# Performance work log

Hardware: AMD Instinct MI355X
Metric: run time of the kernel (lower is better)

The kernel has to match this reference:

```python
import jax, jax.numpy as jnp
import numpy as np
from jax import lax

B, S, V, E, H, L, LAT = 32, 64, 32000, 128, 512, 2, 64

def setup_inputs() -> dict:
    key = jax.random.key(0)
    ks = jax.random.split(key, 40)
    sc = 0.05
    inputs = jax.random.randint(ks[0], (B, S), 0, V, dtype=jnp.int32)
    lengths = jnp.sort(jax.random.randint(ks[1], (B,), 1, S + 1, dtype=jnp.int32))[::-1]
    lengths = lengths.at[0].set(S)  # enforce_sorted=True, max length == S for static shapes
    d = {
        'inputs': inputs,
        'lengths': lengths,
        'noise': jax.random.normal(ks[2], (L, B, LAT), jnp.float32),
        'embed_table': jax.random.normal(ks[3], (V, E), jnp.float32) * sc,
        'enc_Wm': jax.random.normal(ks[4], (LAT, E), jnp.float32) * sc,
        'enc_bm': jnp.zeros((LAT,), jnp.float32),
        'enc_Wv': jax.random.normal(ks[5], (LAT, E), jnp.float32) * sc,
        'enc_bv': jnp.zeros((LAT,), jnp.float32),
        'W_l2r': jax.random.normal(ks[6], (H, LAT), jnp.float32) * sc,
        'b_l2r': jnp.zeros((H,), jnp.float32),
        'gru_Wih0': jax.random.normal(ks[7], (3 * H, E), jnp.float32) * sc,
        'gru_Whh0': jax.random.normal(ks[8], (3 * H, H), jnp.float32) * sc,
        'gru_bih0': jnp.zeros((3 * H,), jnp.float32),
        'gru_bhh0': jnp.zeros((3 * H,), jnp.float32),
        'gru_Wih1': jax.random.normal(ks[9], (3 * H, H), jnp.float32) * sc,
        'gru_Whh1': jax.random.normal(ks[10], (3 * H, H), jnp.float32) * sc,
        'gru_bih1': jnp.zeros((3 * H,), jnp.float32),
        'gru_bhh1': jnp.zeros((3 * H,), jnp.float32),
        'W_out': jax.random.normal(ks[11], (V, H), jnp.float32) * sc,
        'b_out': jnp.zeros((V,), jnp.float32),
        'logp_W1': jax.random.normal(ks[12], (200, LAT), jnp.float32) * sc,
        'logp_b1': jnp.zeros((200,), jnp.float32),
        'logp_W2': jax.random.normal(ks[13], (100, 200), jnp.float32) * sc,
        'logp_b2': jnp.zeros((100,), jnp.float32),
        'logp_W3': jax.random.normal(ks[14], (1, 100), jnp.float32) * sc,
        'logp_b3': jnp.zeros((1,), jnp.float32),
        'sas_W1': jax.random.normal(ks[15], (200, LAT), jnp.float32) * sc,
        'sas_b1': jnp.zeros((200,), jnp.float32),
        'sas_W2': jax.random.normal(ks[16], (100, 200), jnp.float32) * sc,
        'sas_b2': jnp.zeros((100,), jnp.float32),
        'sas_W3': jax.random.normal(ks[17], (1, 100), jnp.float32) * sc,
        'sas_b3': jnp.zeros((1,), jnp.float32),
    }
    return d

def _gru_layer(x, h0, Wih, Whh, bih, bhh, lengths):
    # x: [B,T,D]; PyTorch GRU gate order: r, z, n. Packed semantics: state frozen
    # and output zero beyond each sample's length.
    T = x.shape[1]
    xW = jnp.einsum('btd,gd->btg', x, Wih) + bih          # [B,T,3H] one big GEMM
    tmask = jnp.arange(T)[:, None] < lengths[None, :]      # [T,B]
    def step(h, inp):
        xw_t, m_t = inp                                    # [B,3H], [B]
        hW = h @ Whh.T + bhh
        xr, xz, xn = jnp.split(xw_t, 3, axis=-1)
        hr, hz, hn = jnp.split(hW, 3, axis=-1)
        r = jax.nn.sigmoid(xr + hr)
        u = jax.nn.sigmoid(xz + hz)
        n = jnp.tanh(xn + r * hn)
        h_new = (1.0 - u) * n + u * h
        m = m_t[:, None]
        h = jnp.where(m, h_new, h)
        out = jnp.where(m, h_new, 0.0)
        return h, out
    hT, outs = lax.scan(step, h0, (xW.transpose(1, 0, 2), tmask))
    return outs.transpose(1, 0, 2), hT                     # [B,T,H], [B,H]

def _mlp3(x, W1, b1, W2, b2, W3, b3):
    h = jax.nn.relu(x @ W1.T + b1)
    h = jax.nn.relu(h @ W2.T + b2)
    return (h @ W3.T + b3).reshape(-1)

def reference(inputs, lengths, noise, embed_table, enc_Wm, enc_bm, enc_Wv, enc_bv,
              W_l2r, b_l2r, gru_Wih0, gru_Whh0, gru_bih0, gru_bhh0,
              gru_Wih1, gru_Whh1, gru_bih1, gru_bhh1, W_out, b_out,
              logp_W1, logp_b1, logp_W2, logp_b2, logp_W3, logp_b3,
              sas_W1, sas_b1, sas_W2, sas_b2, sas_W3, sas_b3):
    emb = embed_table[inputs]                              # [B,S,E] gather
    # ragged masked segment-sum: sum embeddings of tokens with id > 2 per sample
    mask = (inputs > 2)[..., None].astype(emb.dtype)
    vec_frag = jnp.sum(emb * mask, axis=1)                 # [B,E]
    mean = vec_frag @ enc_Wm.T + enc_bm                    # [B,LAT]
    logv = vec_frag @ enc_Wv.T + enc_bv
    std = jnp.exp(0.5 * logv)
    z = noise * std + mean                                 # [L,B,LAT]
    pred_logp = _mlp3(mean, logp_W1, logp_b1, logp_W2, logp_b2, logp_W3, logp_b3)
    pred_sas = _mlp3(mean, sas_W1, sas_b1, sas_W2, sas_b2, sas_W3, sas_b3)
    state = z @ W_l2r.T + b_l2r                            # [L,B,H]
    # decoder: 2-layer GRU (eval mode: no dropout), then vocab projection
    out0, _ = _gru_layer(emb, state[0], gru_Wih0, gru_Whh0, gru_bih0, gru_bhh0, lengths)
    out1, _ = _gru_layer(out0, state[1], gru_Wih1, gru_Whh1, gru_bih1, gru_bhh1, lengths)
    output = out1 @ W_out.T + b_out                        # [B,S,V]
    return (output, mean, std, z, pred_logp, pred_sas)
```

## Files before the change

### kernel.cpp

```cpp
#include <hip/hip_runtime.h>


typedef __attribute__((ext_vector_type(8))) short bf16x8_t;
typedef __attribute__((ext_vector_type(8))) unsigned short u16x8_t;
typedef __attribute__((ext_vector_type(4))) float f32x4_t;
typedef __attribute__((ext_vector_type(8))) _Float16 f16x8_t;
typedef __attribute__((ext_vector_type(4))) unsigned int u32x4_t;

#define AS_AGENT __HIP_MEMORY_SCOPE_AGENT

static __device__ __forceinline__ unsigned short f2bf(float f) {
    unsigned int u = __float_as_uint(f);
    u += 0x7fffu + ((u >> 16) & 1u);
    return (unsigned short)(u >> 16);
}
static __device__ __forceinline__ unsigned short bfround(unsigned int u) {
    u += 0x7fffu + ((u >> 16) & 1u);
    return (unsigned short)(u >> 16);
}
static __device__ __forceinline__ unsigned short f2h(float f) {
    _Float16 h = (_Float16)f;
    return __builtin_bit_cast(unsigned short, h);
}
static __device__ __forceinline__ float sigmoidf_(float x) {
    return 1.f / (1.f + __expf(-x));
}

__global__ __launch_bounds__(256) void embed_encoder_kernel(
    const int* __restrict__ tok, const float* __restrict__ table,
    const float* __restrict__ Wih0f,
    const float* __restrict__ Wm, const float* __restrict__ bm,
    const float* __restrict__ Wv, const float* __restrict__ bv,
    const float* __restrict__ noise,
    const float* __restrict__ Wl2r, const float* __restrict__ bl2r,
    const float* __restrict__ lW1, const float* __restrict__ lb1,
    const float* __restrict__ lW2, const float* __restrict__ lb2,
    const float* __restrict__ lW3, const float* __restrict__ lb3,
    const float* __restrict__ sW1, const float* __restrict__ sb1,
    const float* __restrict__ sW2, const float* __restrict__ sb2,
    const float* __restrict__ sW3, const float* __restrict__ sb3,
    float* __restrict__ o_mean, float* __restrict__ o_std, float* __restrict__ o_z,
    float* __restrict__ o_logp, float* __restrict__ o_sas,
    float* __restrict__ state,
    unsigned short* __restrict__ embb,
    unsigned short* __restrict__ Wih0b)
{
    const int b = blockIdx.x, tid = threadIdx.x;
    __shared__ float v_[128], mn[64], sd[64], zz[2][64], hh1[200], hh2[100];
    if (tid < 128) {
        const int e = tid;
        float acc = 0.f;
        for (int s = 0; s < 64; ++s) {
            int id = tok[b * 64 + s];
            float v = table[(size_t)id * 128 + e];
            embb[(size_t)(b * 64 + s) * 128 + e] = f2bf(v);
            if (id > 2) acc += v;
        }
        v_[e] = acc;
    }
    for (int i = b * 256 + tid; i < 49152; i += 8192) {
        float4 v = reinterpret_cast<const float4*>(Wih0f)[i];
        ushort4 o;
        o.x = f2bf(v.x); o.y = f2bf(v.y); o.z = f2bf(v.z); o.w = f2bf(v.w);
        reinterpret_cast<ushort4*>(Wih0b)[i] = o;
    }
    __syncthreads();
    if (tid < 128) {
        int j = tid & 63;
        bool isv = tid >= 64;
        const float* W = (isv ? Wv : Wm) + j * 128;
        float a = isv ? bv[j] : bm[j];
#pragma unroll 4
        for (int k = 0; k < 128; ++k) a = fmaf(v_[k], W[k], a);
        if (!isv) { mn[j] = a; o_mean[b * 64 + j] = a; }
        else      { float s = __expf(0.5f * a); sd[j] = s; o_std[b * 64 + j] = s; }
    }
    __syncthreads();
    if (tid < 128) {
        int l = tid >> 6, j = tid & 63;
        float zv = fmaf(noise[(l * 32 + b) * 64 + j], sd[j], mn[j]);
        zz[l][j] = zv;
        o_z[(l * 32 + b) * 64 + j] = zv;
    }
    __syncthreads();
#pragma unroll
    for (int p = 0; p < 4; ++p) {
        int tt = p * 256 + tid;
        int l = tt >> 9, hd = tt & 511;
        const float* W = Wl2r + hd * 64;
        float a = bl2r[hd];
#pragma unroll 4
        for (int k = 0; k < 64; ++k) a = fmaf(zz[l][k], W[k], a);
        state[(size_t)(l * 32 + b) * 512 + hd] = a;
    }
    if (tid < 200) {
        const float* W = lW1 + tid * 64;
        float a = lb1[tid];
        for (int k = 0; k < 64; ++k) a = fmaf(mn[k], W[k], a);
        hh1[tid] = fmaxf(a, 0.f);
    }
    __syncthreads();
    if (tid < 100) {
        const float* W = lW2 + tid * 200;
        float a = lb2[tid];
        for (int k = 0; k < 200; ++k) a = fmaf(hh1[k], W[k], a);
        hh2[tid] = fmaxf(a, 0.f);
    }
    __syncthreads();
    if (tid == 0) {
        float a = lb3[0];
        for (int k = 0; k < 100; ++k) a = fmaf(hh2[k], lW3[k], a);
        o_logp[b] = a;
    }
    __syncthreads();
    if (tid < 200) {
        const float* W = sW1 + tid * 64;
        float a = sb1[tid];
        for (int k = 0; k < 64; ++k) a = fmaf(mn[k], W[k], a);
        hh1[tid] = fmaxf(a, 0.f);
    }
    __syncthreads();
    if (tid < 100) {
        const float* W = sW2 + tid * 200;
        float a = sb2[tid];
        for (int k = 0; k < 200; ++k) a = fmaf(hh1[k], W[k], a);
        hh2[tid] = fmaxf(a, 0.f);
    }
    __syncthreads();
    if (tid == 0) {
        float a = sb3[0];
        for (int k = 0; k < 100; ++k) a = fmaf(hh2[k], sW3[k], a);
        o_sas[b] = a;
    }
}

#define NWG_L0 16
#define NWG_TOT 48
#define NWG_ALL 256
#define NWG_GEMM 208
#define OCH 32832

__global__ __launch_bounds__(512) void gru_fused_kernel(
    float* __restrict__ xW0,
    const unsigned short* __restrict__ embb,
    const unsigned short* __restrict__ Wih0b,
    const float* __restrict__ bih0,
    const float* __restrict__ Whh0, const float* __restrict__ bhh0,
    const float* __restrict__ Whh1, const float* __restrict__ Wih1,
    const float* __restrict__ bih1, const float* __restrict__ bhh1,
    const float* __restrict__ hinit,
    const int* __restrict__ lengths,
    unsigned short* __restrict__ h0x,
    unsigned short* __restrict__ h1x,
    unsigned short* __restrict__ o0x,
    unsigned short* __restrict__ out1x,
    const float* __restrict__ Woutf,
    unsigned short* __restrict__ Woutb,
    const float* __restrict__ bout,
    float* __restrict__ outp,
    int* __restrict__ flags)
{
    __shared__ __align__(16) char smem[157184];
    const int tid = threadIdx.x;
    const int wg = blockIdx.x;
    const int lane = tid & 63;
    const int wave = tid >> 6;
    unsigned int* __restrict__ h0x32 = (unsigned int*)h0x;
    unsigned int* __restrict__ h1x32 = (unsigned int*)h1x;
    unsigned int* __restrict__ o0x32 = (unsigned int*)o0x;
    unsigned int* __restrict__ o1x32 = (unsigned int*)out1x;

    (void)__hip_atomic_load(&flags[0], __ATOMIC_ACQUIRE, AS_AGENT);

    if (wg >= NWG_TOT) {
        unsigned short* lA = (unsigned short*)smem;
        unsigned short* lB = (unsigned short*)(smem + 16384);
        const int g = wg - NWG_TOT;
        const int wm = wave >> 2;
        const int wn = wave & 3;

        if (g < 192) {
            const int pm = g / 12, pn = g % 12;
            f32x4_t pacc[4][2];
#pragma unroll
            for (int i = 0; i < 4; ++i)
#pragma unroll
                for (int j = 0; j < 2; ++j) pacc[i][j] = (f32x4_t){0.f, 0.f, 0.f, 0.f};
            for (int kt = 0; kt < 128; kt += 64) {
#pragma unroll
                for (int p = 0; p < 2; ++p) {
                    int gi = p * 512 + tid;
                    int row = gi >> 3, c8 = gi & 7;
                    int dst = row * 64 + ((c8 ^ (row & 7)) << 3);
                    *(u32x4_t*)&lA[dst] = *(const u32x4_t*)(embb +
                        (size_t)(pm * 128 + row) * 128 + kt + (c8 << 3));
                    *(u32x4_t*)&lB[dst] = *(const u32x4_t*)(Wih0b +
                        (size_t)(pn * 128 + row) * 128 + kt + (c8 << 3));
                }
                __syncthreads();
#pragma unroll
                for (int kc = 0; kc < 2; ++kc) {
                    int c8 = kc * 4 + (lane >> 4);
                    bf16x8_t af[4], bfr[2];
#pragma unroll
                    for (int i = 0; i < 4; ++i) {
                        int ra = wm * 64 + i * 16 + (lane & 15);
                        af[i] = *(const bf16x8_t*)&lA[ra * 64 + ((c8 ^ (ra & 7)) << 3)];
                    }
#pragma unroll
                    for (int j = 0; j < 2; ++j) {
                        int rb = wn * 32 + j * 16 + (lane & 15);
                        bfr[j] = *(const bf16x8_t*)&lB[rb * 64 + ((c8 ^ (rb & 7)) << 3)];
                    }
#pragma unroll
                    for (int i = 0; i < 4; ++i)
#pragma unroll
                        for (int j = 0; j < 2; ++j)
                            pacc[i][j] = __builtin_amdgcn_mfma_f32_16x16x32_bf16(
                                af[i], bfr[j], pacc[i][j], 0, 0, 0);
                }
                __syncthreads();
            }
            const int lm = (lane >> 4) * 4, ln = lane & 15;
#pragma unroll
            for (int i = 0; i < 4; ++i) {
#pragma unroll
                for (int j = 0; j < 2; ++j) {
                    int gn = pn * 128 + wn * 32 + j * 16 + ln;
                    float bb_ = bih0[gn];
#pragma unroll
                    for (int r = 0; r < 4; ++r) {
                        int gm = pm * 128 + wm * 64 + i * 16 + lm + r;
                        __hip_atomic_store(&xW0[(size_t)gm * 1536 + gn],
                                           pacc[i][j][r] + bb_, __ATOMIC_RELAXED, AS_AGENT);
                    }
                }
            }
            asm volatile("s_waitcnt vmcnt(0)" ::: "memory");
            __syncthreads();
            if (tid == 0)
                __hip_atomic_store(&flags[8192 + g * 16], 1, __ATOMIC_RELAXED, AS_AGENT);
        }

        for (int pn = g; pn < 250; pn += NWG_GEMM) {
            const u32x4_t* src = (const u32x4_t*)Woutf + (size_t)pn * 16384;
            unsigned long long* dst = (unsigned long long*)Woutb + (size_t)pn * 16384;
            for (int i = tid; i < 16384; i += 512) {
                u32x4_t q = __builtin_nontemporal_load(src + i);
                unsigned int lo = (unsigned int)bfround(q[0]) | ((unsigned int)bfround(q[1]) << 16);
                unsigned int hi = (unsigned int)bfround(q[2]) | ((unsigned int)bfround(q[3]) << 16);
                unsigned long long w = (unsigned long long)lo | ((unsigned long long)hi << 32);
                __hip_atomic_store(dst + i, w, __ATOMIC_RELAXED, AS_AGENT);
            }
            asm volatile("s_waitcnt vmcnt(0)" ::: "memory");
            __syncthreads();
            if (tid == 0)
                __hip_atomic_store(&flags[2048 + pn * 16], 1, __ATOMIC_RELAXED, AS_AGENT);
        }

        int mPrev = -1;
        for (int T = g; T < 4000; T += NWG_GEMM) {
            const int m = T / 250, n = T % 250;
            if (m != mPrev) {
                if (wave == 0) {
                    const int tgt = 4 * m + 6;
                    for (;;) {
                        int v = 0x40000000;
                        if (lane < 32)
                            v = __hip_atomic_load(&flags[(NWG_L0 + lane) << 5],
                                                  __ATOMIC_RELAXED, AS_AGENT);
                        if (__all(v >= tgt)) break;
                        __builtin_amdgcn_s_sleep(8);
                    }
                }
                mPrev = m;
            }
            if (wave == 0) {
                while (__hip_atomic_load(&flags[2048 + n * 16], __ATOMIC_RELAXED, AS_AGENT) < 1)
                    __builtin_amdgcn_s_sleep(8);
            }
            __syncthreads();

            f32x4_t acc[4][2];
#pragma unroll
            for (int i = 0; i < 4; ++i)
#pragma unroll
                for (int j = 0; j < 2; ++j) acc[i][j] = (f32x4_t){0.f, 0.f, 0.f, 0.f};

            for (int kt = 0; kt < 512; kt += 64) {
#pragma unroll
                for (int p = 0; p < 2; ++p) {
                    int gi = p * 512 + tid;
                    int row = gi >> 3, c8 = gi & 7;
                    int dst = row * 64 + ((c8 ^ (row & 7)) << 3);
                    u32x4_t qa = *(const u32x4_t*)(out1x + (size_t)m * 65664 +
                                                   row * 512 + kt + (c8 << 3));
                    u32x4_t qb = *(const u32x4_t*)(Woutb + ((size_t)(n * 128 + row)) * 512 +
                                                   kt + (c8 << 3));
                    *(u32x4_t*)&lA[dst] = qa;
                    *(u32x4_t*)&lB[dst] = qb;
                }
                __syncthreads();
#pragma unroll
                for (int kc = 0; kc < 2; ++kc) {
                    bf16x8_t af[4], bfr[2];
                    int c8 = kc * 4 + (lane >> 4);
#pragma unroll
                    for (int i = 0; i < 4; ++i) {
                        int ra = wm * 64 + i * 16 + (lane & 15);
                        af[i] = *(const bf16x8_t*)&lA[ra * 64 + ((c8 ^ (ra & 7)) << 3)];
                    }
#pragma unroll
                    for (int j = 0; j < 2; ++j) {
                        int rb = wn * 32 + j * 16 + (lane & 15);
                        bfr[j] = *(const bf16x8_t*)&lB[rb * 64 + ((c8 ^ (rb & 7)) << 3)];
                    }
#pragma unroll
                    for (int i = 0; i < 4; ++i)
#pragma unroll
                        for (int j = 0; j < 2; ++j)
                            acc[i][j] = __builtin_amdgcn_mfma_f32_16x16x32_bf16(
                                af[i], bfr[j], acc[i][j], 0, 0, 0);
                }
                __syncthreads();
            }
            const int lm = (lane >> 4) * 4, ln = lane & 15;
#pragma unroll
            for (int i = 0; i < 4; ++i) {
                int rl0 = wm * 64 + i * 16 + lm;
#pragma unroll
                for (int j = 0; j < 2; ++j) {
                    int gn = n * 128 + wn * 32 + j * 16 + ln;
                    float bb = bout[gn];
#pragma unroll
                    for (int r = 0; r < 4; ++r) {
                        int rl = rl0 + r;
                        int t = 4 * m + (rl >> 5), b = rl & 31;
                        __builtin_nontemporal_store(acc[i][j][r] + bb,
                            &outp[(size_t)(b * 64 + t) * 32000 + gn]);
                    }
                }
            }
        }
        return;
    }

    unsigned short* Wl = (unsigned short*)smem;
    u32x4_t* hstage4 = (u32x4_t*)(smem + 98304);
    float* csm = (float*)(smem + 131072);
#define CSM(p, gt, b, c) csm[((((p)*3 + (gt)) * 32 + (b)) * 34) + (c)]
    const int gate = wave >> 1;
    const int mt = wave & 1;

    if (wg < NWG_L0) {
        const int d0 = wg * 32;
        for (int idx = tid; idx < 6144; idx += 512) {
            int ln = idx & 63, kk = (idx >> 6) & 15, nt = (idx >> 10) & 1, g_ = idx >> 11;
            int grow = g_ * 512 + d0 + nt * 16 + (ln & 15);
            int k = kk * 32 + ((ln >> 4) << 3);
            const float* src = Whh0 + (size_t)grow * 512 + k;
            f16x8_t v;
#pragma unroll
            for (int j = 0; j < 8; ++j) v[j] = (_Float16)src[j];
            *(f16x8_t*)&Wl[idx << 3] = v;
        }
        const int ub = tid >> 4, dpl = (tid & 15) * 2, ud = d0 + dpl;
        float h_lo = hinit[(size_t)ub * 512 + ud];
        float h_hi = hinit[(size_t)ub * 512 + ud + 1];
        const float br_lo = bhh0[ud],        br_hi = bhh0[ud + 1];
        const float bz_lo = bhh0[512 + ud],  bz_hi = bhh0[512 + ud + 1];
        const float bn_lo = bhh0[1024 + ud], bn_hi = bhh0[1024 + ud + 1];
        const int lenb = lengths[ub];
        {
            unsigned int hw = (unsigned int)f2h(h_lo) | ((unsigned int)f2h(h_hi) << 16);
            __hip_atomic_store(&h0x32[ub * 256 + (ud >> 1)], hw, __ATOMIC_RELAXED, AS_AGENT);
        }
        asm volatile("s_waitcnt vmcnt(0)" ::: "memory");
        __syncthreads();
        if (tid == 0) __hip_atomic_store(&flags[wg << 5], 1, __ATOMIC_RELAXED, AS_AGENT);

        if (wave == 0) {
            for (;;) {
                int mnv = 1;
#pragma unroll
                for (int bb = 0; bb < 3; ++bb) {
                    int idx = bb * 64 + lane;
                    if (idx < 192) {
                        int v = __hip_atomic_load(&flags[8192 + idx * 16],
                                                  __ATOMIC_RELAXED, AS_AGENT);
                        mnv = v < mnv ? v : mnv;
                    }
                }
                if (__all(mnv >= 1)) break;
                __builtin_amdgcn_s_sleep(2);
            }
        }
        __syncthreads();

        const float* xrow = xW0 + (size_t)(ub * 64) * 1536 + ud;
        float2 px_r = *(const float2*)(xrow);
        float2 px_z = *(const float2*)(xrow + 512);
        float2 px_n = *(const float2*)(xrow + 1024);

        for (int r = 0; r < 64; ++r) {
            if (wave == 0) {
                for (;;) {
                    int v = 0x40000000;
                    int tgt = (lane < NWG_L0) ? (r + 1) : (r - 2);
                    if (lane < NWG_TOT)
                        v = __hip_atomic_load(&flags[lane << 5], __ATOMIC_RELAXED, AS_AGENT);
                    else
                        tgt = 0;
                    if (__all(v >= tgt)) break;
                    __builtin_amdgcn_s_sleep(1);
                }
            }
            __syncthreads();
            {
                const char* srcb = (const char*)h0x + ((r & 1) << 15);
                u32x4_t q0, q1, q2, q3;
                asm volatile("global_load_dwordx4 %0, %1, off sc0 sc1"
                             : "=v"(q0) : "v"(srcb + ((size_t)tid << 4)) : "memory");
                asm volatile("global_load_dwordx4 %0, %1, off sc0 sc1"
                             : "=v"(q1) : "v"(srcb + ((size_t)(512 + tid) << 4)) : "memory");
                asm volatile("global_load_dwordx4 %0, %1, off sc0 sc1"
                             : "=v"(q2) : "v"(srcb + ((size_t)(1024 + tid) << 4)) : "memory");
                asm volatile("global_load_dwordx4 %0, %1, off sc0 sc1"
                             : "=v"(q3) : "v"(srcb + ((size_t)(1536 + tid) << 4)) : "memory");
                asm volatile("s_waitcnt vmcnt(0)" ::: "memory");
                int g0 = tid, g1 = 512 + tid, g2 = 1024 + tid, g3 = 1536 + tid;
                hstage4[g0 ^ ((g0 >> 6) & 7)] = q0;
                hstage4[g1 ^ ((g1 >> 6) & 7)] = q1;
                hstage4[g2 ^ ((g2 >> 6) & 7)] = q2;
                hstage4[g3 ^ ((g3 >> 6) & 7)] = q3;
            }
            __syncthreads();
            if (wave < 6) {
                const int brow = mt * 16 + (lane & 15);
                const int ko = lane >> 4;
                f32x4_t acc0 = (f32x4_t){0.f, 0.f, 0.f, 0.f};
                f32x4_t acc1 = (f32x4_t){0.f, 0.f, 0.f, 0.f};
#pragma unroll
                for (int kk = 0; kk < 16; ++kk) {
                    int gg = brow * 64 + kk * 4 + ko;
                    f16x8_t af = __builtin_bit_cast(f16x8_t, hstage4[gg ^ (brow & 7)]);
                    f16x8_t bf0 = *(const f16x8_t*)&Wl[(((gate * 2 + 0) * 16 + kk) * 64 + lane) << 3];
                    f16x8_t bf1 = *(const f16x8_t*)&Wl[(((gate * 2 + 1) * 16 + kk) * 64 + lane) << 3];
                    acc0 = __builtin_amdgcn_mfma_f32_16x16x32_f16(af, bf0, acc0, 0, 0, 0);
                    acc1 = __builtin_amdgcn_mfma_f32_16x16x32_f16(af, bf1, acc1, 0, 0, 0);
                }
                const int crow = mt * 16 + ((lane >> 4) << 2), ccol = lane & 15;
#pragma unroll
                for (int rr = 0; rr < 4; ++rr) {
                    CSM(0, gate, crow + rr, ccol) = acc0[rr];
                    CSM(0, gate, crow + rr, 16 + ccol) = acc1[rr];
                }
            }
            __syncthreads();
            unsigned int ow = 0u;
            if (r < lenb) {
                float hr_lo = CSM(0, 0, ub, dpl), hr_hi = CSM(0, 0, ub, dpl + 1);
                float hz_lo = CSM(0, 1, ub, dpl), hz_hi = CSM(0, 1, ub, dpl + 1);
                float hn_lo = CSM(0, 2, ub, dpl), hn_hi = CSM(0, 2, ub, dpl + 1);
                float r0 = sigmoidf_(px_r.x + hr_lo + br_lo);
                float r1 = sigmoidf_(px_r.y + hr_hi + br_hi);
                float u0 = sigmoidf_(px_z.x + hz_lo + bz_lo);
                float u1 = sigmoidf_(px_z.y + hz_hi + bz_hi);
                float n0 = tanhf(px_n.x + r0 * (hn_lo + bn_lo));
                float n1 = tanhf(px_n.y + r1 * (hn_hi + bn_hi));
                h_lo = (1.f - u0) * n0 + u0 * h_lo;
                h_hi = (1.f - u1) * n1 + u1 * h_hi;
                ow = (unsigned int)f2h(h_lo) | ((unsigned int)f2h(h_hi) << 16);
            }
            {
                unsigned int hw = (unsigned int)f2h(h_lo) | ((unsigned int)f2h(h_hi) << 16);
                __hip_atomic_store(&h0x32[((r + 1) & 1) * 8192 + ub * 256 + (ud >> 1)],
                                   hw, __ATOMIC_RELAXED, AS_AGENT);
                __hip_atomic_store(&o0x32[(r & 3) * 8192 + ub * 256 + (ud >> 1)],
                                   ow, __ATOMIC_RELAXED, AS_AGENT);
            }
            asm volatile("s_waitcnt vmcnt(0)" ::: "memory");
            __syncthreads();
            if (tid == 0) __hip_atomic_store(&flags[wg << 5], r + 2, __ATOMIC_RELAXED, AS_AGENT);
            {
                int tn = r + 1 < 64 ? r + 1 : 63;
                const float* xp = xW0 + (size_t)(ub * 64 + tn) * 1536 + ud;
                px_r = *(const float2*)(xp);
                px_z = *(const float2*)(xp + 512);
                px_n = *(const float2*)(xp + 1024);
            }
        }
    } else {
        const int lid = wg - NWG_L0;
        const int d0 = lid * 16;
        for (int idx = tid; idx < 6144; idx += 512) {
            int ln = idx & 63, kk = (idx >> 6) & 31, g_ = idx >> 11;
            int grow = g_ * 512 + d0 + (ln & 15);
            int k = (kk & 15) * 32 + ((ln >> 4) << 3);
            const float* src = (kk < 16 ? Whh1 : Wih1) + (size_t)grow * 512 + k;
            f16x8_t v;
#pragma unroll
            for (int j = 0; j < 8; ++j) v[j] = (_Float16)src[j];
            *(f16x8_t*)&Wl[idx << 3] = v;
        }
        const bool upd = (tid < 256);
        const int ub = tid >> 3, dpl = (tid & 7) * 2, ud = d0 + dpl;
        float h_lo = 0.f, h_hi = 0.f;
        float br_lo = 0.f, br_hi = 0.f, bz_lo = 0.f, bz_hi = 0.f;
        float bxn_lo = 0.f, bxn_hi = 0.f, bhn_lo = 0.f, bhn_hi = 0.f;
        int lenb = 0;
        if (upd) {
            h_lo = hinit[16384 + (size_t)ub * 512 + ud];
            h_hi = hinit[16384 + (size_t)ub * 512 + ud + 1];
            br_lo = bih1[ud] + bhh1[ud];
            br_hi = bih1[ud + 1] + bhh1[ud + 1];
            bz_lo = bih1[512 + ud] + bhh1[512 + ud];
            bz_hi = bih1[512 + ud + 1] + bhh1[512 + ud + 1];
            bxn_lo = bih1[1024 + ud];   bxn_hi = bih1[1024 + ud + 1];
            bhn_lo = bhh1[1024 + ud];   bhn_hi = bhh1[1024 + ud + 1];
            lenb = lengths[ub];
            unsigned int hw = (unsigned int)f2h(h_lo) | ((unsigned int)f2h(h_hi) << 16);
            __hip_atomic_store(&h1x32[8192 + ub * 256 + (ud >> 1)], hw, __ATOMIC_RELAXED, AS_AGENT);
        }
        asm volatile("s_waitcnt vmcnt(0)" ::: "memory");
        __syncthreads();
        if (tid == 0) __hip_atomic_store(&flags[wg << 5], 2, __ATOMIC_RELAXED, AS_AGENT);

        for (int r = 1; r <= 64; ++r) {
            const int t1 = r - 1;
            if (wave == 0) {
                const int tgt = r + 1;
                for (;;) {
                    int v = 0x40000000;
                    if (lane < NWG_TOT)
                        v = __hip_atomic_load(&flags[lane << 5], __ATOMIC_RELAXED, AS_AGENT);
                    if (__all(v >= tgt)) break;
                    __builtin_amdgcn_s_sleep(1);
                }
            }
            __syncthreads();
            u32x4_t a0, a1, a2, a3, b0, b1, b2, b3;
            {
                const char* sh = (const char*)h1x + ((r & 1) << 15);
                const char* so = (const char*)o0x + ((t1 & 3) << 15);
                asm volatile("global_load_dwordx4 %0, %1, off sc0 sc1"
                             : "=v"(a0) : "v"(sh + ((size_t)tid << 4)) : "memory");
                asm volatile("global_load_dwordx4 %0, %1, off sc0 sc1"
                             : "=v"(a1) : "v"(sh + ((size_t)(512 + tid) << 4)) : "memory");
                asm volatile("global_load_dwordx4 %0, %1, off sc0 sc1"
                             : "=v"(a2) : "v"(sh + ((size_t)(1024 + tid) << 4)) : "memory");
                asm volatile("global_load_dwordx4 %0, %1, off sc0 sc1"
                             : "=v"(a3) : "v"(sh + ((size_t)(1536 + tid) << 4)) : "memory");
                asm volatile("global_load_dwordx4 %0, %1, off sc0 sc1"
                             : "=v"(b0) : "v"(so + ((size_t)tid << 4)) : "memory");
                asm volatile("global_load_dwordx4 %0, %1, off sc0 sc1"
                             : "=v"(b1) : "v"(so + ((size_t)(512 + tid) << 4)) : "memory");
                asm volatile("global_load_dwordx4 %0, %1, off sc0 sc1"
                             : "=v"(b2) : "v"(so + ((size_t)(1024 + tid) << 4)) : "memory");
                asm volatile("global_load_dwordx4 %0, %1, off sc0 sc1"
                             : "=v"(b3) : "v"(so + ((size_t)(1536 + tid) << 4)) : "memory");
                asm volatile("s_waitcnt vmcnt(4)" ::: "memory");
                int g0 = tid, g1 = 512 + tid, g2 = 1024 + tid, g3 = 1536 + tid;
                hstage4[g0 ^ ((g0 >> 6) & 7)] = a0;
                hstage4[g1 ^ ((g1 >> 6) & 7)] = a1;
                hstage4[g2 ^ ((g2 >> 6) & 7)] = a2;
                hstage4[g3 ^ ((g3 >> 6) & 7)] = a3;
            }
            __syncthreads();
            f32x4_t acc_h = (f32x4_t){0.f, 0.f, 0.f, 0.f};
            const int brow = mt * 16 + (lane & 15);
            const int ko = lane >> 4;
            if (wave < 6) {
#pragma unroll
                for (int kk = 0; kk < 16; ++kk) {
                    int gg = brow * 64 + kk * 4 + ko;
                    f16x8_t af = __builtin_bit_cast(f16x8_t, hstage4[gg ^ (brow & 7)]);
                    f16x8_t bf = *(const f16x8_t*)&Wl[(((gate * 32 + kk) * 64 + lane)) << 3];
                    acc_h = __builtin_amdgcn_mfma_f32_16x16x32_f16(af, bf, acc_h, 0, 0, 0);
                }
            }
            __syncthreads();
            {
                asm volatile("s_waitcnt vmcnt(0)" ::: "memory");
                int g0 = tid, g1 = 512 + tid, g2 = 1024 + tid, g3 = 1536 + tid;
                hstage4[g0 ^ ((g0 >> 6) & 7)] = b0;
                hstage4[g1 ^ ((g1 >> 6) & 7)] = b1;
                hstage4[g2 ^ ((g2 >> 6) & 7)] = b2;
                hstage4[g3 ^ ((g3 >> 6) & 7)] = b3;
            }
            __syncthreads();
            if (wave < 6) {
                f32x4_t acc_x = (f32x4_t){0.f, 0.f, 0.f, 0.f};
#pragma unroll
                for (int kk = 0; kk < 16; ++kk) {
                    int gg = brow * 64 + kk * 4 + ko;
                    f16x8_t af = __builtin_bit_cast(f16x8_t, hstage4[gg ^ (brow & 7)]);
                    f16x8_t bf = *(const f16x8_t*)&Wl[(((gate * 32 + 16 + kk) * 64 + lane)) << 3];
                    acc_x = __builtin_amdgcn_mfma_f32_16x16x32_f16(af, bf, acc_x, 0, 0, 0);
                }
                const int crow = mt * 16 + ((lane >> 4) << 2), ccol = lane & 15;
#pragma unroll
                for (int rr = 0; rr < 4; ++rr) {
                    CSM(0, gate, crow + rr, ccol) = acc_h[rr];
                    CSM(1, gate, crow + rr, ccol) = acc_x[rr];
                }
            }
            __syncthreads();
            unsigned int ow = 0u;
            if (upd) {
                if (t1 < lenb) {
                    float hr_lo = CSM(0, 0, ub, dpl), hr_hi = CSM(0, 0, ub, dpl + 1);
                    float hz_lo = CSM(0, 1, ub, dpl), hz_hi = CSM(0, 1, ub, dpl + 1);
                    float hn_lo = CSM(0, 2, ub, dpl), hn_hi = CSM(0, 2, ub, dpl + 1);
                    float xr_lo = CSM(1, 0, ub, dpl), xr_hi = CSM(1, 0, ub, dpl + 1);
                    float xz_lo = CSM(1, 1, ub, dpl), xz_hi = CSM(1, 1, ub, dpl + 1);
                    float xn_lo = CSM(1, 2, ub, dpl), xn_hi = CSM(1, 2, ub, dpl + 1);
                    float r0 = sigmoidf_(xr_lo + hr_lo + br_lo);
                    float r1 = sigmoidf_(xr_hi + hr_hi + br_hi);
                    float u0 = sigmoidf_(xz_lo + hz_lo + bz_lo);
                    float u1 = sigmoidf_(xz_hi + hz_hi + bz_hi);
                    float n0 = tanhf(xn_lo + bxn_lo + r0 * (hn_lo + bhn_lo));
                    float n1 = tanhf(xn_hi + bxn_hi + r1 * (hn_hi + bhn_hi));
                    h_lo = (1.f - u0) * n0 + u0 * h_lo;
                    h_hi = (1.f - u1) * n1 + u1 * h_hi;
                    ow = (unsigned int)f2bf(h_lo) | ((unsigned int)f2bf(h_hi) << 16);
                }
                if (r < 64) {
                    unsigned int hw = (unsigned int)f2h(h_lo) | ((unsigned int)f2h(h_hi) << 16);
                    __hip_atomic_store(&h1x32[((r + 1) & 1) * 8192 + ub * 256 + (ud >> 1)],
                                       hw, __ATOMIC_RELAXED, AS_AGENT);
                }
                __hip_atomic_store(&o1x32[(size_t)(t1 >> 2) * OCH +
                                          ((t1 & 3) * 32 + ub) * 256 + (ud >> 1)],
                                   ow, __ATOMIC_RELAXED, AS_AGENT);
            }
            asm volatile("s_waitcnt vmcnt(0)" ::: "memory");
            __syncthreads();
            if (tid == 0)
                __hip_atomic_store(&flags[wg << 5], r + 2, __ATOMIC_RELAXED, AS_AGENT);
        }
    }
#undef CSM
}

extern "C" void kernel_launch(void* const* d_in, const int* in_sizes, int n_in,
                              void* d_out, int out_size, void* d_ws, size_t ws_size,
                              hipStream_t stream) {
    const int*   tok    = (const int*)d_in[0];
    const int*   lens   = (const int*)d_in[1];
    const float* noise  = (const float*)d_in[2];
    const float* table  = (const float*)d_in[3];
    const float* Wm     = (const float*)d_in[4];
    const float* bm_    = (const float*)d_in[5];
    const float* Wv     = (const float*)d_in[6];
    const float* bv_    = (const float*)d_in[7];
    const float* Wl2r   = (const float*)d_in[8];
    const float* bl2r   = (const float*)d_in[9];
    const float* Wih0   = (const float*)d_in[10];
    const float* Whh0   = (const float*)d_in[11];
    const float* bih0   = (const float*)d_in[12];
    const float* bhh0   = (const float*)d_in[13];
    const float* Wih1   = (const float*)d_in[14];
    const float* Whh1   = (const float*)d_in[15];
    const float* bih1   = (const float*)d_in[16];
    const float* bhh1   = (const float*)d_in[17];
    const float* Wout   = (const float*)d_in[18];
    const float* bout   = (const float*)d_in[19];
    const float* lW1 = (const float*)d_in[20]; const float* lb1 = (const float*)d_in[21];
    const float* lW2 = (const float*)d_in[22]; const float* lb2 = (const float*)d_in[23];
    const float* lW3 = (const float*)d_in[24]; const float* lb3 = (const float*)d_in[25];
    const float* sW1 = (const float*)d_in[26]; const float* sb1 = (const float*)d_in[27];
    const float* sW2 = (const float*)d_in[28]; const float* sb2 = (const float*)d_in[29];
    const float* sW3 = (const float*)d_in[30]; const float* sb3 = (const float*)d_in[31];

    float* out    = (float*)d_out;
    float* o_mean = out + 65536000;
    float* o_std  = o_mean + 2048;
    float* o_z    = o_std + 2048;
    float* o_logp = o_z + 4096;
    float* o_sas  = o_logp + 32;

    char* ws = (char*)d_ws;
    unsigned short* Woutb = (unsigned short*)ws;  ws += 32768000;
    unsigned short* Wih0b = (unsigned short*)ws;  ws += 393216;
    unsigned short* embb  = (unsigned short*)ws;  ws += 524288;
    float*          state = (float*)ws;           ws += 131072;
    float*          xW    = (float*)ws;           ws += 12582912;
    unsigned short* out1x = (unsigned short*)ws;  ws += 2101248;
    unsigned short* h0x   = (unsigned short*)ws;  ws += 131072;
    unsigned short* h1x   = (unsigned short*)ws;  ws += 131072;
    unsigned short* o0x   = (unsigned short*)ws;  ws += 262144;
    int*            flgp  = (int*)ws;             ws += 65536;

    (void)hipMemsetAsync(flgp, 0, 65536, stream);

    embed_encoder_kernel<<<dim3(32), dim3(256), 0, stream>>>(
        tok, table, Wih0, Wm, bm_, Wv, bv_, noise, Wl2r, bl2r,
        lW1, lb1, lW2, lb2, lW3, lb3, sW1, sb1, sW2, sb2, sW3, sb3,
        o_mean, o_std, o_z, o_logp, o_sas, state, embb, Wih0b);

    gru_fused_kernel<<<dim3(NWG_ALL), dim3(512), 0, stream>>>(
        xW, embb, Wih0b, bih0, Whh0, bhh0, Whh1, Wih1, bih1, bhh1, state, lens,
        h0x, h1x, o0x, out1x, Wout, Woutb, bout, out, flgp);
}
```

Baseline: 347.3 us.

## Fold embed/encoder kernel into persistent GRU kernel with flag-based dependencies

Removes the separate embed/encoder launch and runs its work inside the persistent GRU kernel. GEMM workgroups 0-31 do the per-batch embedding gather, encoder, MLP heads and state projection, and workgroups 32-63 convert Wih0 to bf16. Each publishes a flag when done, and the input-projection GEMM and both GRU layers spin on these flags before using the data. This drops one kernel launch and its serialization gap, in exchange for extra work and spin-waits on the critical path inside the fused kernel.

```diff
diff --git a/kernel.cpp b/kernel.cpp
--- a/kernel.cpp
+++ b/kernel.cpp
@@ -26,9 +26,14 @@
     return 1.f / (1.f + __expf(-x));
 }
 
-__global__ __launch_bounds__(256) void embed_encoder_kernel(
+#define NWG_L0 16
+#define NWG_TOT 48
+#define NWG_ALL 256
+#define NWG_GEMM 208
+#define OCH 32832
+
+__global__ __launch_bounds__(512) void gru_fused_kernel(
     const int* __restrict__ tok, const float* __restrict__ table,
-    const float* __restrict__ Wih0f,
     const float* __restrict__ Wm, const float* __restrict__ bm,
     const float* __restrict__ Wv, const float* __restrict__ bv,
     const float* __restrict__ noise,
@@ -39,125 +44,23 @@
     const float* __restrict__ sW1, const float* __restrict__ sb1,
     const float* __restrict__ sW2, const float* __restrict__ sb2,
     const float* __restrict__ sW3, const float* __restrict__ sb3,
-    float* __restrict__ o_mean, float* __restrict__ o_std, float* __restrict__ o_z,
-    float* __restrict__ o_logp, float* __restrict__ o_sas,
-    float* __restrict__ state,
-    unsigned short* __restrict__ embb,
-    unsigned short* __restrict__ Wih0b)
-{
-    const int b = blockIdx.x, tid = threadIdx.x;
-    __shared__ float v_[128], mn[64], sd[64], zz[2][64], hh1[200], hh2[100];
-    if (tid < 128) {
-        const int e = tid;
-        float acc = 0.f;
-        for (int s = 0; s < 64; ++s) {
-            int id = tok[b * 64 + s];
-            float v = table[(size_t)id * 128 + e];
-            embb[(size_t)(b * 64 + s) * 128 + e] = f2bf(v);
-            if (id > 2) acc += v;
-        }
-        v_[e] = acc;
-    }
-    for (int i = b * 256 + tid; i < 49152; i += 8192) {
-        float4 v = reinterpret_cast<const float4*>(Wih0f)[i];
-        ushort4 o;
-        o.x = f2bf(v.x); o.y = f2bf(v.y); o.z = f2bf(v.z); o.w = f2bf(v.w);
-        reinterpret_cast<ushort4*>(Wih0b)[i] = o;
-    }
-    __syncthreads();
-    if (tid < 128) {
-        int j = tid & 63;
-        bool isv = tid >= 64;
-        const float* W = (isv ? Wv : Wm) + j * 128;
-        float a = isv ? bv[j] : bm[j];
-#pragma unroll 4
-        for (int k = 0; k < 128; ++k) a = fmaf(v_[k], W[k], a);
-        if (!isv) { mn[j] = a; o_mean[b * 64 + j] = a; }
-        else      { float s = __expf(0.5f * a); sd[j] = s; o_std[b * 64 + j] = s; }
-    }
-    __syncthreads();
-    if (tid < 128) {
-        int l = tid >> 6, j = tid & 63;
-        float zv = fmaf(noise[(l * 32 + b) * 64 + j], sd[j], mn[j]);
-        zz[l][j] = zv;
-        o_z[(l * 32 + b) * 64 + j] = zv;
-    }
-    __syncthreads();
-#pragma unroll
-    for (int p = 0; p < 4; ++p) {
-        int tt = p * 256 + tid;
-        int l = tt >> 9, hd = tt & 511;
-        const float* W = Wl2r + hd * 64;
-        float a = bl2r[hd];
-#pragma unroll 4
-        for (int k = 0; k < 64; ++k) a = fmaf(zz[l][k], W[k], a);
-        state[(size_t)(l * 32 + b) * 512 + hd] = a;
-    }
-    if (tid < 200) {
-        const float* W = lW1 + tid * 64;
-        float a = lb1[tid];
-        for (int k = 0; k < 64; ++k) a = fmaf(mn[k], W[k], a);
-        hh1[tid] = fmaxf(a, 0.f);
-    }
-    __syncthreads();
-    if (tid < 100) {
-        const float* W = lW2 + tid * 200;
-        float a = lb2[tid];
-        for (int k = 0; k < 200; ++k) a = fmaf(hh1[k], W[k], a);
-        hh2[tid] = fmaxf(a, 0.f);
-    }
-    __syncthreads();
-    if (tid == 0) {
-        float a = lb3[0];
-        for (int k = 0; k < 100; ++k) a = fmaf(hh2[k], lW3[k], a);
-        o_logp[b] = a;
-    }
-    __syncthreads();
-    if (tid < 200) {
-        const float* W = sW1 + tid * 64;
-        float a = sb1[tid];
-        for (int k = 0; k < 64; ++k) a = fmaf(mn[k], W[k], a);
-        hh1[tid] = fmaxf(a, 0.f);
-    }
-    __syncthreads();
-    if (tid < 100) {
-        const float* W = sW2 + tid * 200;
-        float a = sb2[tid];
-        for (int k = 0; k < 200; ++k) a = fmaf(hh1[k], W[k], a);
-        hh2[tid] = fmaxf(a, 0.f);
-    }
-    __syncthreads();
-    if (tid == 0) {
-        float a = sb3[0];
-        for (int k = 0; k < 100; ++k) a = fmaf(hh2[k], sW3[k], a);
-        o_sas[b] = a;
-    }
-}
-
-#define NWG_L0 16
-#define NWG_TOT 48
-#define NWG_ALL 256
-#define NWG_GEMM 208
-#define OCH 32832
-
-__global__ __launch_bounds__(512) void gru_fused_kernel(
-    float* __restrict__ xW0,
-    const unsigned short* __restrict__ embb,
-    const unsigned short* __restrict__ Wih0b,
-    const float* __restrict__ bih0,
+    const float* __restrict__ Wih0f, const float* __restrict__ bih0,
     const float* __restrict__ Whh0, const float* __restrict__ bhh0,
     const float* __restrict__ Whh1, const float* __restrict__ Wih1,
     const float* __restrict__ bih1, const float* __restrict__ bhh1,
-    const float* __restrict__ hinit,
     const int* __restrict__ lengths,
+    const float* __restrict__ Woutf, const float* __restrict__ bout,
+    float* __restrict__ outp,
+    float* __restrict__ aux,
+    unsigned short* __restrict__ embb,
+    unsigned short* __restrict__ Wih0b,
+    float* __restrict__ state,
+    float* __restrict__ xW0,
     unsigned short* __restrict__ h0x,
     unsigned short* __restrict__ h1x,
     unsigned short* __restrict__ o0x,
     unsigned short* __restrict__ out1x,
-    const float* __restrict__ Woutf,
     unsigned short* __restrict__ Woutb,
-    const float* __restrict__ bout,
-    float* __restrict__ outp,
     int* __restrict__ flags)
 {
     __shared__ __align__(16) char smem[157184];
@@ -179,7 +82,133 @@
         const int wm = wave >> 2;
         const int wn = wave & 3;
 
+        if (g < 32) {
+            const int b = g;
+            float* v_  = (float*)smem;
+            float* mn  = v_ + 128;
+            float* sd  = mn + 64;
+            float* zz  = sd + 64;
+            float* hh1 = zz + 128;
+            float* hh2 = hh1 + 200;
+            float* o_mean = aux, *o_std = aux + 2048, *o_z = aux + 4096;
+            float* o_logp = aux + 8192, *o_sas = aux + 8224;
+            if (tid < 128) {
+                const int e = tid;
+                float acc = 0.f;
+                for (int s = 0; s < 64; ++s) {
+                    int id = tok[b * 64 + s];
+                    float v = table[(size_t)id * 128 + e];
+                    __hip_atomic_store(&embb[(size_t)(b * 64 + s) * 128 + e],
+                                       f2bf(v), __ATOMIC_RELAXED, AS_AGENT);
+                    if (id > 2) acc += v;
+                }
+                v_[e] = acc;
+            }
+            __syncthreads();
+            if (tid < 128) {
+                int j = tid & 63;
+                bool isv = tid >= 64;
+                const float* W = (isv ? Wv : Wm) + j * 128;
+                float a = isv ? bv[j] : bm[j];
+#pragma unroll 4
+                for (int k = 0; k < 128; ++k) a = fmaf(v_[k], W[k], a);
+                if (!isv) { mn[j] = a; o_mean[b * 64 + j] = a; }
+                else      { float s = __expf(0.5f * a); sd[j] = s; o_std[b * 64 + j] = s; }
+            }
+            __syncthreads();
+            if (tid < 128) {
+                int l = tid >> 6, j = tid & 63;
+                float zv = fmaf(noise[(l * 32 + b) * 64 + j], sd[j], mn[j]);
+                zz[l * 64 + j] = zv;
+                o_z[(l * 32 + b) * 64 + j] = zv;
+            }
+            __syncthreads();
+#pragma unroll
+            for (int p = 0; p < 2; ++p) {
+                int tt = p * 512 + tid;
+                int l = tt >> 9, hd = tt & 511;
+                const float* W = Wl2r + hd * 64;
+                float a = bl2r[hd];
+#pragma unroll 4
+                for (int k = 0; k < 64; ++k) a = fmaf(zz[l * 64 + k], W[k], a);
+                __hip_atomic_store(&state[(size_t)(l * 32 + b) * 512 + hd],
+                                   a, __ATOMIC_RELAXED, AS_AGENT);
+            }
+            if (tid < 200) {
+                const float* W = lW1 + tid * 64;
+                float a = lb1[tid];
+                for (int k = 0; k < 64; ++k) a = fmaf(mn[k], W[k], a);
+                hh1[tid] = fmaxf(a, 0.f);
+            }
+            __syncthreads();
+            if (tid < 100) {
+                const float* W = lW2 + tid * 200;
+                float a = lb2[tid];
+                for (int k = 0; k < 200; ++k) a = fmaf(hh1[k], W[k], a);
+                hh2[tid] = fmaxf(a, 0.f);
+            }
+            __syncthreads();
+            if (tid == 0) {
+                float a = lb3[0];
+                for (int k = 0; k < 100; ++k) a = fmaf(hh2[k], lW3[k], a);
+                o_logp[b] = a;
+            }
+            __syncthreads();
+            if (tid < 200) {
+                const float* W = sW1 + tid * 64;
+                float a = sb1[tid];
+                for (int k = 0; k < 64; ++k) a = fmaf(mn[k], W[k], a);
+                hh1[tid] = fmaxf(a, 0.f);
+            }
+            __syncthreads();
+            if (tid < 100) {
+                const float* W = sW2 + tid * 200;
+                float a = sb2[tid];
+                for (int k = 0; k < 200; ++k) a = fmaf(hh1[k], W[k], a);
+                hh2[tid] = fmaxf(a, 0.f);
+            }
+            __syncthreads();
+            if (tid == 0) {
+                float a = sb3[0];
+                for (int k = 0; k < 100; ++k) a = fmaf(hh2[k], sW3[k], a);
+                o_sas[b] = a;
+            }
+            asm volatile("s_waitcnt vmcnt(0)" ::: "memory");
+            __syncthreads();
+            if (tid == 0)
+                __hip_atomic_store(&flags[12288 + b * 16], 1, __ATOMIC_RELAXED, AS_AGENT);
+        }
+        if (g >= 32 && g < 64) {
+            const int j = g - 32;
+            for (int i = j * 1536 + tid; i < (j + 1) * 1536; i += 512) {
+                float4 v = reinterpret_cast<const float4*>(Wih0f)[i];
+                unsigned int lo = (unsigned int)f2bf(v.x) | ((unsigned int)f2bf(v.y) << 16);
+                unsigned int hi = (unsigned int)f2bf(v.z) | ((unsigned int)f2bf(v.w) << 16);
+                unsigned long long w = (unsigned long long)lo | ((unsigned long long)hi << 32);
+                __hip_atomic_store((unsigned long long*)Wih0b + i, w, __ATOMIC_RELAXED, AS_AGENT);
+            }
+            asm volatile("s_waitcnt vmcnt(0)" ::: "memory");
+            __syncthreads();
+            if (tid == 0)
+                __hip_atomic_store(&flags[13312 + j * 16], 1, __ATOMIC_RELAXED, AS_AGENT);
+        }
+
         if (g < 192) {
+            if (wave == 0) {
+                for (;;) {
+                    int v = 1;
+                    if (lane < 32) {
+                        int e = __hip_atomic_load(&flags[12288 + lane * 16],
+                                                  __ATOMIC_RELAXED, AS_AGENT);
+                        int c = __hip_atomic_load(&flags[13312 + lane * 16],
+                                                  __ATOMIC_RELAXED, AS_AGENT);
+                        v = e < c ? e : c;
+                    }
+                    if (__all(v >= 1)) break;
+                    __builtin_amdgcn_s_sleep(2);
+                }
+            }
+            __syncthreads();
             const int pm = g / 12, pn = g % 12;
             f32x4_t pacc[4][2];
 #pragma unroll
@@ -364,9 +393,19 @@
             for (int j = 0; j < 8; ++j) v[j] = (_Float16)src[j];
             *(f16x8_t*)&Wl[idx << 3] = v;
         }
+        if (wave == 0) {
+            for (;;) {
+                int v = 1;
+                if (lane < 32) v = __hip_atomic_load(&flags[12288 + lane * 16],
+                                                     __ATOMIC_RELAXED, AS_AGENT);
+                if (__all(v >= 1)) break;
+                __builtin_amdgcn_s_sleep(2);
+            }
+        }
+        __syncthreads();
         const int ub = tid >> 4, dpl = (tid & 15) * 2, ud = d0 + dpl;
-        float h_lo = hinit[(size_t)ub * 512 + ud];
-        float h_hi = hinit[(size_t)ub * 512 + ud + 1];
+        float h_lo = state[(size_t)ub * 512 + ud];
+        float h_hi = state[(size_t)ub * 512 + ud + 1];
         const float br_lo = bhh0[ud],        br_hi = bhh0[ud + 1];
         const float bz_lo = bhh0[512 + ud],  bz_hi = bhh0[512 + ud + 1];
         const float bn_lo = bhh0[1024 + ud], bn_hi = bhh0[1024 + ud + 1];
@@ -503,6 +542,16 @@
             for (int j = 0; j < 8; ++j) v[j] = (_Float16)src[j];
             *(f16x8_t*)&Wl[idx << 3] = v;
         }
+        if (wave == 0) {
+            for (;;) {
+                int v = 1;
+                if (lane < 32) v = __hip_atomic_load(&flags[12288 + lane * 16],
+                                                     __ATOMIC_RELAXED, AS_AGENT);
+                if (__all(v >= 1)) break;
+                __builtin_amdgcn_s_sleep(2);
+            }
+        }
+        __syncthreads();
         const bool upd = (tid < 256);
         const int ub = tid >> 3, dpl = (tid & 7) * 2, ud = d0 + dpl;
         float h_lo = 0.f, h_hi = 0.f;
@@ -510,8 +559,8 @@
         float bxn_lo = 0.f, bxn_hi = 0.f, bhn_lo = 0.f, bhn_hi = 0.f;
         int lenb = 0;
         if (upd) {
-            h_lo = hinit[16384 + (size_t)ub * 512 + ud];
-            h_hi = hinit[16384 + (size_t)ub * 512 + ud + 1];
+            h_lo = state[16384 + (size_t)ub * 512 + ud];
+            h_hi = state[16384 + (size_t)ub * 512 + ud + 1];
             br_lo = bih1[ud] + bhh1[ud];
             br_hi = bih1[ud + 1] + bhh1[ud + 1];
             bz_lo = bih1[512 + ud] + bhh1[512 + ud];
@@ -673,12 +722,8 @@
     const float* sW2 = (const float*)d_in[28]; const float* sb2 = (const float*)d_in[29];
     const float* sW3 = (const float*)d_in[30]; const float* sb3 = (const float*)d_in[31];
 
-    float* out    = (float*)d_out;
-    float* o_mean = out + 65536000;
-    float* o_std  = o_mean + 2048;
-    float* o_z    = o_std + 2048;
-    float* o_logp = o_z + 4096;
-    float* o_sas  = o_logp + 32;
+    float* out = (float*)d_out;
+    float* aux = out + 65536000;
 
     char* ws = (char*)d_ws;
     unsigned short* Woutb = (unsigned short*)ws;  ws += 32768000;
@@ -694,12 +739,10 @@
 
     (void)hipMemsetAsync(flgp, 0, 65536, stream);
 
-    embed_encoder_kernel<<<dim3(32), dim3(256), 0, stream>>>(
-        tok, table, Wih0, Wm, bm_, Wv, bv_, noise, Wl2r, bl2r,
+    gru_fused_kernel<<<dim3(NWG_ALL), dim3(512), 0, stream>>>(
+        tok, table, Wm, bm_, Wv, bv_, noise, Wl2r, bl2r,
         lW1, lb1, lW2, lb2, lW3, lb3, sW1, sb1, sW2, sb2, sW3, sb3,
-        o_mean, o_std, o_z, o_logp, o_sas, state, embb, Wih0b);
-
-    gru_fused_kernel<<<dim3(NWG_ALL), dim3(512), 0, stream>>>(
-        xW, embb, Wih0b, bih0, Whh0, bhh0, Whh1, Wih1, bih1, bhh1, state, lens,
-        h0x, h1x, o0x, out1x, Wout, Woutb, bout, out, flgp);
+        Wih0, bih0, Whh0, bhh0, Whh1, Wih1, bih1, bhh1, lens,
+        Wout, bout, out, aux, embb, Wih0b, state, xW,
+        h0x, h1x, o0x, out1x, Woutb, flgp);
 }
```

New measurement: 354.7 us. +2.1%, slower.
